# Kernel tuning notes

Hardware: AMD Instinct MI355X
Metric: run time of the kernel (lower is better)

Reference implementation:

```python
import jax, jax.numpy as jnp
import numpy as np

B, F, H, T = 32, 128, 256, 2048


def setup_inputs() -> dict:
    key = jax.random.key(0)
    ks = jax.random.split(key, 20)
    s = 0.05
    x = jax.random.normal(ks[0], (B, 1, T, F), dtype=jnp.float32)
    mask = (jax.random.uniform(ks[1], (B, 1, T, F)) < 0.5).astype(jnp.float32)
    delta = jax.random.uniform(ks[2], (B, 1, T, F), dtype=jnp.float32)  # time since last obs
    inp = jnp.concatenate([x, mask, delta], axis=1)  # [B, 3, T, F]
    p = lambda k, shape: jax.random.normal(k, shape, dtype=jnp.float32) * s
    return {
        "input": inp,
        "x_mean": p(ks[3], (F,)),
        # layer 0: input decay (diagonal), hidden decay, gates
        "w_dx": p(ks[4], (F,)), "b_dx": p(ks[5], (F,)),
        "W_dh0": p(ks[6], (F, H)), "b_dh0": p(ks[7], (H,)),
        "W0": p(ks[8], (F, 3 * H)), "U0": p(ks[9], (H, 3 * H)),
        "V0": p(ks[10], (F, 3 * H)), "b0": p(ks[11], (3 * H,)),
        # layer 1: hidden decay from delta, gates (input = prev layer hidden)
        "W_dh1": p(ks[12], (F, H)), "b_dh1": p(ks[13], (H,)),
        "W1": p(ks[14], (H, 3 * H)), "U1": p(ks[15], (H, 3 * H)),
        "V1": p(ks[16], (F, 3 * H)), "b1": p(ks[17], (3 * H,)),
    }


def _grud_cell(x_in, m, delta, h, W_dh, b_dh, W, U, V, b):
    # hidden-state decay from delta-time
    gamma_h = jnp.exp(-jax.nn.relu(delta @ W_dh + b_dh))  # [B,H]
    h = gamma_h * h
    pre = x_in @ W + m @ V + b                             # [B,3H]
    hU = h @ U[:, : 2 * H]                                 # r,z recurrent terms
    r = jax.nn.sigmoid(pre[:, :H] + hU[:, :H])
    z = jax.nn.sigmoid(pre[:, H : 2 * H] + hU[:, H : 2 * H])
    h_tilde = jnp.tanh(pre[:, 2 * H :] + (r * h) @ U[:, 2 * H :])
    return (1.0 - z) * h + z * h_tilde


def reference(input, x_mean, w_dx, b_dx, W_dh0, b_dh0, W0, U0, V0, b0,
              W_dh1, b_dh1, W1, U1, V1, b1):
    xs = jnp.moveaxis(input, 2, 0)  # [T, B, 3, F]
    x_last0 = jnp.broadcast_to(x_mean, (B, F))
    h0 = jnp.zeros((B, H), dtype=input.dtype)
    h1 = jnp.zeros((B, H), dtype=input.dtype)

    def step(carry, inp_t):
        x_last, h0, h1 = carry
        x, m, delta = inp_t[:, 0], inp_t[:, 1], inp_t[:, 2]  # [B,F] each
        # input decay toward empirical mean (GRU-D imputation)
        gamma_x = jnp.exp(-jax.nn.relu(delta * w_dx + b_dx))
        x_hat = m * x + (1.0 - m) * (gamma_x * x_last + (1.0 - gamma_x) * x_mean)
        h0n = _grud_cell(x_hat, m, delta, h0, W_dh0, b_dh0, W0, U0, V0, b0)
        h1n = _grud_cell(h0n, m, delta, h1, W_dh1, b_dh1, W1, U1, V1, b1)
        x_last_new = jnp.where(m > 0, x, x_last)  # update AFTER the cells, as in torch
        return (x_last_new, h0n, h1n), h1n

    _, ys = jax.lax.scan(step, (x_last0, h0, h1), xs)
    return ys  # [T, B, H]
```

## Files before the change

### kernel.cpp

```cpp
#include <hip/hip_runtime.h>

typedef _Float16 f16;
typedef _Float16 f16x2 __attribute__((ext_vector_type(2)));
typedef unsigned int u32;

#define CB 32
#define CF 128
#define CH 256
#define CT 2048
#define TCC 128
#define SEG 16
#define SLEN 128
#define SHBYTES 150784

static __device__ __forceinline__ f16x2 bc(u32 u){ return __builtin_bit_cast(f16x2, u); }
static __device__ __forceinline__ u32 packh2(float lo, float hi){ f16x2 v; v.x=(f16)lo; v.y=(f16)hi; return __builtin_bit_cast(u32, v); }

static __device__ __forceinline__ float dot2f(f16x2 a, f16x2 b, float c){
#if defined(__has_builtin)
#if __has_builtin(__builtin_amdgcn_fdot2)
  return __builtin_amdgcn_fdot2(a, b, c, false);
#else
  return c + (float)a.x*(float)b.x + (float)a.y*(float)b.y;
#endif
#else
  return c + (float)a.x*(float)b.x + (float)a.y*(float)b.y;
#endif
}
static __device__ __forceinline__ float dot4q(float acc, uint4 w, uint4 h){
  acc = dot2f(bc(w.x), bc(h.x), acc);
  acc = dot2f(bc(w.y), bc(h.y), acc);
  acc = dot2f(bc(w.z), bc(h.z), acc);
  acc = dot2f(bc(w.w), bc(h.w), acc);
  return acc;
}
#define DOT4V(ACC, BASE, H) { \
  ACC = dot2f(bc(wv[(BASE)+0]), bc((H).x), ACC); \
  ACC = dot2f(bc(wv[(BASE)+1]), bc((H).y), ACC); \
  ACC = dot2f(bc(wv[(BASE)+2]), bc((H).z), ACC); \
  ACC = dot2f(bc(wv[(BASE)+3]), bc((H).w), ACC); }

__global__ void init_hst(float* hst){
  int i = blockIdx.x*256 + threadIdx.x;
  if (i < 2*CB*CH) hst[i] = 0.f;
}

static __device__ __forceinline__ float wc0src(int k, int n, const float* W0, const float* V0, const float* Wdh0){
  if (k < 128) return (n < 768) ? W0[k*768 + n] : 0.f;
  if (k < 256) return (n < 768) ? V0[(k-128)*768 + n] : 0.f;
  return (n >= 768) ? Wdh0[(k-256)*256 + (n-768)] : 0.f;
}
static __device__ __forceinline__ float wc1src(int k, int n, const float* W1, const float* V1, const float* Wdh1){
  if (k < 256) return (n < 768) ? W1[k*768 + n] : 0.f;
  if (k < 384) return (n < 768) ? V1[(k-256)*768 + n] : 0.f;
  return (n >= 768) ? Wdh1[(k-384)*256 + (n-768)] : 0.f;
}
static __device__ __forceinline__ u32 wrz_pair(int flat, int jj, int L, const float* U){
  int p = L >> 2, q = L & 3;
  int cc = flat >> 3, j = flat & 7;
  int col = 4*p + cc;
  int pr = 32*q + 4*j + jj;
  return packh2(U[(2*pr)*768 + col], U[(2*pr+1)*768 + col]);
}
static __device__ __forceinline__ u32 wcc_pair(int flat, int jj, int L, const float* U){
  int p = L >> 2, q = L & 3;
  int cc2 = flat >> 3, j = flat & 7;
  int col = 512 + 2*p + cc2;
  int pr = 32*q + 4*j + jj;
  return packh2(U[(2*pr)*768 + col], U[(2*pr+1)*768 + col]);
}
static __device__ __forceinline__ u32 wrv_src(int v, int L, const float* U){
  if (v < 56) return wrz_pair(v >> 2, v & 3, L, U);
  if (v < 88){ int u = v - 56; return wcc_pair(u >> 2, u & 3, L, U); }
  int u = v - 88;
  return wrz_pair(26 + (u >> 2), u & 3, L, U);
}
static __device__ __forceinline__ u32 wrl_src(int g, int jj, int L, const float* U){
  if (g < 12) return wrz_pair(14 + g, jj, L, U);
  return wcc_pair(8 + (g - 12), jj, L, U);
}
static __device__ __forceinline__ u32 wrg_src(int g, int jj, int L, const float* U){
  if (g < 3) return wrz_pair(29 + g, jj, L, U);
  return wcc_pair(14 + (g - 3), jj, L, U);
}

__global__ __launch_bounds__(256) void pack_w(
    const float* __restrict__ W0, const float* __restrict__ V0, const float* __restrict__ Wdh0,
    const float* __restrict__ W1, const float* __restrict__ V1, const float* __restrict__ Wdh1,
    const float* __restrict__ U0, const float* __restrict__ U1,
    const float* __restrict__ b0, const float* __restrict__ bdh0,
    const float* __restrict__ b1, const float* __restrict__ bdh1,
    u32* __restrict__ WC0p, u32* __restrict__ WC1p,
    u32* __restrict__ WRVa, u32* __restrict__ WRVb,
    u32* __restrict__ WRLa, u32* __restrict__ WRLb,
    u32* __restrict__ WRGa, u32* __restrict__ WRGb,
    float* __restrict__ bias0, float* __restrict__ bias1){
  int idx = blockIdx.x*256 + threadIdx.x;
  if (idx < 196608){
    int k2 = idx >> 10, n = idx & 1023;
    WC0p[idx] = packh2(wc0src(2*k2, n, W0,V0,Wdh0), wc0src(2*k2+1, n, W0,V0,Wdh0));
  } else if (idx < 458752){
    int j = idx - 196608; int k2 = j >> 10, n = j & 1023;
    WC1p[j] = packh2(wc1src(2*k2, n, W1,V1,Wdh1), wc1src(2*k2+1, n, W1,V1,Wdh1));
  } else if (idx < 509952){
    int j = idx - 458752; int v = j >> 9, L = j & 511;
    WRVa[j] = wrv_src(v, L, U0);
  } else if (idx < 561152){
    int j = idx - 509952; int v = j >> 9, L = j & 511;
    WRVb[j] = wrv_src(v, L, U1);
  } else if (idx < 598016){
    int j = idx - 561152; int g = j >> 11, L = (j >> 2) & 511, jj = j & 3;
    WRLa[j] = wrl_src(g, jj, L, U0);
  } else if (idx < 634880){
    int j = idx - 598016; int g = j >> 11, L = (j >> 2) & 511, jj = j & 3;
    WRLb[j] = wrl_src(g, jj, L, U1);
  } else if (idx < 645120){
    int j = idx - 634880; int g = j >> 11, L = (j >> 2) & 511, jj = j & 3;
    WRGa[j] = wrg_src(g, jj, L, U0);
  } else if (idx < 655360){
    int j = idx - 645120; int g = j >> 11, L = (j >> 2) & 511, jj = j & 3;
    WRGb[j] = wrg_src(g, jj, L, U1);
  } else if (idx < 657408){
    int i = idx - 655360;
    if (i < 1024) bias0[i] = (i < 768) ? b0[i] : bdh0[i - 768];
    else { int j = i - 1024; bias1[j] = (j < 768) ? b1[j] : bdh1[j - 768]; }
  }
}

__global__ __launch_bounds__(256) void k1a(const float* __restrict__ in,
    float* __restrict__ segval, int* __restrict__ seghas){
  int tid = blockIdx.x*256 + threadIdx.x;
  int s = tid >> 12, chain = tid & 4095;
  int b = chain >> 7, f = chain & 127;
  const float* px = in + ((size_t)b*3 + 0)*CT*CF + f;
  const float* pm = in + ((size_t)b*3 + 1)*CT*CF + f;
  float last = 0.f; int has = 0;
  #pragma unroll 4
  for (int u = 0; u < SLEN; ++u){
    int t = s*SLEN + u;
    float m = pm[(size_t)t*CF], x = px[(size_t)t*CF];
    if (m > 0.f){ last = x; has = 1; }
  }
  segval[s*4096 + chain] = last;
  seghas[s*4096 + chain] = has;
}
__global__ __launch_bounds__(256) void k1b(const float* __restrict__ x_mean,
    const float* __restrict__ segval, const int* __restrict__ seghas, float* __restrict__ seed){
  int chain = blockIdx.x*256 + threadIdx.x;
  int f = chain & 127;
  float cur = x_mean[f];
  #pragma unroll
  for (int s = 0; s < SEG; ++s){
    seed[s*4096 + chain] = cur;
    if (seghas[s*4096 + chain]) cur = segval[s*4096 + chain];
  }
}
__global__ __launch_bounds__(256) void k1c(const float* __restrict__ in, const float* __restrict__ x_mean,
    const float* __restrict__ w_dx, const float* __restrict__ b_dx,
    const float* __restrict__ seed, f16* __restrict__ A){
  int tid = blockIdx.x*256 + threadIdx.x;
  int s = tid >> 12, chain = tid & 4095;
  int b = chain >> 7, f = chain & 127;
  const float wd = w_dx[f], bd = b_dx[f], xm = x_mean[f];
  const float* px = in + ((size_t)b*3 + 0)*CT*CF + f;
  const float* pm = in + ((size_t)b*3 + 1)*CT*CF + f;
  const float* pd = in + ((size_t)b*3 + 2)*CT*CF + f;
  float xl = seed[s*4096 + chain];
  #pragma unroll 4
  for (int u = 0; u < SLEN; ++u){
    int t = s*SLEN + u;
    float x = px[(size_t)t*CF], m = pm[(size_t)t*CF], d = pd[(size_t)t*CF];
    float gx = __expf(-fmaxf(d*wd + bd, 0.f));
    float xh = m*x + (1.f-m)*(gx*xl + (1.f-gx)*xm);
    f16* wq = A + ((size_t)t*CB + b)*384 + f;
    wq[0] = (f16)xh; wq[128] = (f16)m; wq[256] = (f16)d;
    xl = (m > 0.f) ? x : xl;
  }
}

static __device__ void gemm_tile(
    const u32* __restrict__ Aa, int lda, const u32* __restrict__ Ab, int ldb, int kasplit,
    int ktiles, const u32* __restrict__ Wp, const float* __restrict__ bias, float* __restrict__ Out,
    int row0, int n0, int tid, char* sm){
  u32 (*AsT)[68] = (u32 (*)[68])sm;
  u32 (*Bs)[64]  = (u32 (*)[64])(sm + 4352);
  const int tx = tid & 15, ty = tid >> 4;
  const int am = tid >> 2, akq = (tid & 3) * 4;
  const int bk = tid >> 4, bnq = (tid & 15) * 4;
  float acc[4][4] = {};
  for (int kt = 0; kt < ktiles; ++kt){
    int k2g = kt*16 + akq;
    uint4 ga;
    if (k2g < kasplit) ga = *(const uint4*)&Aa[(size_t)(row0 + am)*lda + k2g];
    else               ga = *(const uint4*)&Ab[(size_t)(row0 + am)*ldb + (k2g - kasplit)];
    uint4 gb = *(const uint4*)&Wp[(size_t)(kt*16 + bk)*1024 + n0 + bnq];
    __syncthreads();
    AsT[akq+0][am] = ga.x; AsT[akq+1][am] = ga.y; AsT[akq+2][am] = ga.z; AsT[akq+3][am] = ga.w;
    *(uint4*)&Bs[bk][bnq] = gb;
    __syncthreads();
    #pragma unroll
    for (int kk = 0; kk < 16; ++kk){
      uint4 bq = *(const uint4*)&Bs[kk][tx*4];
      uint4 aq = *(const uint4*)&AsT[kk][ty*4];
      f16x2 bv0 = bc(bq.x), bv1 = bc(bq.y), bv2 = bc(bq.z), bv3 = bc(bq.w);
      f16x2 av0 = bc(aq.x), av1 = bc(aq.y), av2 = bc(aq.z), av3 = bc(aq.w);
      acc[0][0] = dot2f(av0, bv0, acc[0][0]); acc[0][1] = dot2f(av0, bv1, acc[0][1]);
      acc[0][2] = dot2f(av0, bv2, acc[0][2]); acc[0][3] = dot2f(av0, bv3, acc[0][3]);
      acc[1][0] = dot2f(av1, bv0, acc[1][0]); acc[1][1] = dot2f(av1, bv1, acc[1][1]);
      acc[1][2] = dot2f(av1, bv2, acc[1][2]); acc[1][3] = dot2f(av1, bv3, acc[1][3]);
      acc[2][0] = dot2f(av2, bv0, acc[2][0]); acc[2][1] = dot2f(av2, bv1, acc[2][1]);
      acc[2][2] = dot2f(av2, bv2, acc[2][2]); acc[2][3] = dot2f(av2, bv3, acc[2][3]);
      acc[3][0] = dot2f(av3, bv0, acc[3][0]); acc[3][1] = dot2f(av3, bv1, acc[3][1]);
      acc[3][2] = dot2f(av3, bv2, acc[3][2]); acc[3][3] = dot2f(av3, bv3, acc[3][3]);
    }
  }
  const bool isg = (n0 >= 768);
  #pragma unroll
  for (int i = 0; i < 4; ++i){
    int r = row0 + ty*4 + i;
    int n = n0 + tx*4;
    float4 v;
    float* vv = (float*)&v;
    #pragma unroll
    for (int j = 0; j < 4; ++j){
      float x = acc[i][j] + bias[n + j];
      if (isg) x = __expf(-fmaxf(x, 0.f));
      vv[j] = x;
    }
    *(float4*)&Out[(size_t)r*1024 + n] = v;
  }
}

__global__ __launch_bounds__(512) void mega(
    const float* __restrict__ O0r, const float* __restrict__ O1r,
    const u32* __restrict__ WRVa, const u32* __restrict__ WRVb,
    const u32* __restrict__ WRLa, const u32* __restrict__ WRLb,
    const u32* __restrict__ WRGa, const u32* __restrict__ WRGb,
    float* __restrict__ hst, f16* __restrict__ h0cw, float* __restrict__ out,
    int t0_l1, int n0, int n1, int g0n, int g1n,
    const u32* __restrict__ g0a, float* __restrict__ g0out,
    const u32* __restrict__ g1a, const u32* __restrict__ g1b, float* __restrict__ g1out,
    const u32* __restrict__ WC0p, const u32* __restrict__ WC1p,
    const float* __restrict__ bias0, const float* __restrict__ bias1){
  extern __shared__ __align__(16) char smraw[];
  const int L = threadIdx.x;
  if (blockIdx.x >= 64){
    int gb = blockIdx.x - 64;
    int st = L >> 8, t2 = L & 255;
    char* smst = smraw + st*8448;
    if (gb < g0n){
      int tile = gb*2 + st;
      gemm_tile(g0a, 192, g0a, 192, 192, 12, WC0p, bias0, g0out, (tile>>4)*64, (tile&15)*64, t2, smst);
    } else {
      int tile = (gb - g0n)*2 + st;
      gemm_tile(g1a, 128, g1b, 192, 128, 16, WC1p, bias1, g1out, (tile>>4)*64, (tile&15)*64, t2, smst);
    }
    return;
  }
  const int role = blockIdx.x >> 5;
  const int b = blockIdx.x & 31;
  const int steps = role ? n1 : n0;
  if (steps == 0) return;
  const float* O = role ? O1r : O0r;
  const u32* WRV = role ? WRVb : WRVa;
  const u32* WRL = role ? WRLb : WRLa;
  const u32* WRG = role ? WRGb : WRGa;
  float* hcarry = hst + role*CB*CH;

  uint4* WL   = (uint4*)smraw;
  f16*  hdh_  = (f16*)(smraw + 147456);
  f16*  rh_   = (f16*)(smraw + 148096);
  float* hdf  = (float*)(smraw + 148736);
  float* zz   = (float*)(smraw + 149760);

  #pragma unroll
  for (int g = 0; g < 18; ++g) WL[g*512 + L] = *(const uint4*)&WRL[((size_t)g*512 + L)*4];
  u32 wv[100];
  #pragma unroll
  for (int i = 0; i < 100; ++i) wv[i] = WRV[i*512 + L];

  const int p = L >> 2, q = L & 3;
  size_t row = (size_t)b*1024;
  if (L < 256){
    float hd = O[row + 768 + L] * hcarry[b*256 + L];
    hdf[L] = hd; hdh_[(L>>6)*80 + (L&63)] = (f16)hd;
  }
  float prz = O[row + L];
  const int e2 = 2*p + (q & 1);
  float pc = (q < 2) ? O[row + 512 + e2] : 0.f;
  const char* hqb = (const char*)hdh_ + q*160;
  const char* rqb = (const char*)rh_ + q*160;
  __syncthreads();

  for (int lt = 0; lt < steps; ++lt){
    size_t nrow = row + (size_t)CB*1024;
    float nprz = 0.f, npc = 0.f, ngex = 0.f;
    if (lt + 1 < steps){
      nprz = O[nrow + L];
      if (q < 2){ npc = O[nrow + 512 + e2]; ngex = O[nrow + 768 + e2]; }
    }
    float a0=0.f, a1=0.f, a2=0.f, a3=0.f;
    #pragma unroll
    for (int j = 0; j < 8; ++j){
      uint4 h = ((const uint4*)hqb)[j];
      DOT4V(a0, 4*j, h);
      if (j < 6){ DOT4V(a1, 32 + 4*j, h); }
      else { uint4 wq = WL[(j-6)*512 + L]; a1 = dot4q(a1, wq, h); }
      { uint4 wq = WL[(2+j)*512 + L]; a2 = dot4q(a2, wq, h); }
      if (j < 2){ uint4 wq = WL[(10+j)*512 + L]; a3 = dot4q(a3, wq, h); }
      else if (j < 5){ DOT4V(a3, 88 + 4*(j-2), h); }
      else { uint4 wq = *(const uint4*)&WRG[((size_t)((j-5)*512) + L)*4]; a3 = dot4q(a3, wq, h); }
    }
    a0 += __shfl_xor(a0, 1); a1 += __shfl_xor(a1, 1); a2 += __shfl_xor(a2, 1); a3 += __shfl_xor(a3, 1);
    a0 += __shfl_xor(a0, 2); a1 += __shfl_xor(a1, 2); a2 += __shfl_xor(a2, 2); a3 += __shfl_xor(a3, 2);
    float sum1 = (q == 0) ? a0 : (q == 1) ? a1 : (q == 2) ? a2 : a3;
    float s1 = 1.f/(1.f + __expf(-(sum1 + prz)));
    if (L < 256) rh_[(L>>6)*80 + (L&63)] = (f16)(s1 * hdf[L]);
    else zz[L - 256] = s1;
    __syncthreads();
    float b0_=0.f, b1_=0.f;
    #pragma unroll
    for (int j = 0; j < 8; ++j){
      uint4 r = ((const uint4*)rqb)[j];
      DOT4V(b0_, 56 + 4*j, r);
      if (j < 6){ uint4 wq = WL[(12+j)*512 + L]; b1_ = dot4q(b1_, wq, r); }
      else { uint4 wq = *(const uint4*)&WRG[((size_t)((3+(j-6))*512) + L)*4]; b1_ = dot4q(b1_, wq, r); }
    }
    b0_ += __shfl_xor(b0_, 1); b1_ += __shfl_xor(b1_, 1);
    b0_ += __shfl_xor(b0_, 2); b1_ += __shfl_xor(b1_, 2);
    if (q < 2){
      float sumc = (q & 1) ? b1_ : b0_;
      float v = pc + sumc;
      float e = __expf(2.f*v);
      float ct = 1.f - 2.f/(1.f + e);
      float z = zz[e2];
      float hd = hdf[e2];
      float hn = hd + z*(ct - hd);
      float hdn = ngex*hn;
      hdf[e2] = hdn; hdh_[(e2>>6)*80 + (e2&63)] = (f16)hdn;
      if (role == 0) h0cw[((size_t)lt*CB + b)*256 + e2] = (f16)hn;
      else           out[((size_t)(t0_l1 + lt)*CB + b)*256 + e2] = hn;
      if (lt == steps-1) hcarry[b*256 + e2] = hn;
    }
    prz = nprz; pc = npc;
    row = nrow;
    __syncthreads();
  }
}

extern "C" void kernel_launch(void* const* d_in, const int* in_sizes, int n_in,
                              void* d_out, int out_size, void* d_ws, size_t ws_size,
                              hipStream_t stream){
  const float* input  = (const float*)d_in[0];
  const float* x_mean = (const float*)d_in[1];
  const float* w_dx   = (const float*)d_in[2];
  const float* b_dx   = (const float*)d_in[3];
  const float* Wdh0   = (const float*)d_in[4];
  const float* bdh0   = (const float*)d_in[5];
  const float* W0     = (const float*)d_in[6];
  const float* U0     = (const float*)d_in[7];
  const float* V0     = (const float*)d_in[8];
  const float* b0     = (const float*)d_in[9];
  const float* Wdh1   = (const float*)d_in[10];
  const float* bdh1   = (const float*)d_in[11];
  const float* W1     = (const float*)d_in[12];
  const float* U1     = (const float*)d_in[13];
  const float* V1     = (const float*)d_in[14];
  const float* b1     = (const float*)d_in[15];
  float* out = (float*)d_out;

  hipFuncSetAttribute((const void*)mega, hipFuncAttributeMaxDynamicSharedMemorySize, SHBYTES);

  char* base = (char*)d_ws;
  size_t off = 0;
  auto take = [&](size_t bytes)->char*{
    char* p = base + off;
    off = (off + bytes + 255) & ~(size_t)255;
    return p;
  };
  f16*  IN0h  = (f16*) take((size_t)CT*CB*384*2);
  u32*  WC0p  = (u32*) take((size_t)192*1024*4);
  u32*  WC1p  = (u32*) take((size_t)256*1024*4);
  u32*  WRVa  = (u32*) take((size_t)100*512*4);
  u32*  WRVb  = (u32*) take((size_t)100*512*4);
  u32*  WRLa  = (u32*) take((size_t)18*512*16);
  u32*  WRLb  = (u32*) take((size_t)18*512*16);
  u32*  WRGa  = (u32*) take((size_t)5*512*16);
  u32*  WRGb  = (u32*) take((size_t)5*512*16);
  float* bias0= (float*)take(1024*4);
  float* bias1= (float*)take(1024*4);
  float* hst  = (float*)take((size_t)2*CB*CH*4);
  float* segv = (float*)take((size_t)SEG*4096*4);
  int*   segh = (int*)  take((size_t)SEG*4096*4);
  float* seed = (float*)take((size_t)SEG*4096*4);
  float* O0b[2], *O1b[2]; f16* h0b[2];
  O0b[0] = (float*)take((size_t)TCC*CB*1024*4);
  O0b[1] = (float*)take((size_t)TCC*CB*1024*4);
  O1b[0] = (float*)take((size_t)TCC*CB*1024*4);
  O1b[1] = (float*)take((size_t)TCC*CB*1024*4);
  h0b[0] = (f16*)  take((size_t)TCC*CB*CH*2);
  h0b[1] = (f16*)  take((size_t)TCC*CB*CH*2);

  hipLaunchKernelGGL(init_hst, dim3(64), dim3(256), 0, stream, hst);
  hipLaunchKernelGGL(pack_w, dim3((657408 + 255)/256), dim3(256), 0, stream,
      W0, V0, Wdh0, W1, V1, Wdh1, U0, U1, b0, bdh0, b1, bdh1,
      WC0p, WC1p, WRVa, WRVb, WRLa, WRLb, WRGa, WRGb, bias0, bias1);
  hipLaunchKernelGGL(k1a, dim3(256), dim3(256), 0, stream, input, segv, segh);
  hipLaunchKernelGGL(k1b, dim3(16), dim3(256), 0, stream, x_mean, segv, segh, seed);
  hipLaunchKernelGGL(k1c, dim3(256), dim3(256), 0, stream, input, x_mean, w_dx, b_dx, seed, IN0h);

  const u32* IN0p = (const u32*)IN0h;
  const int nch = CT / TCC;
  for (int i = -1; i <= nch + 1; ++i){
    int r0 = (i >= 0 && i < nch) ? 1 : 0;
    int r1 = (i >= 2 && i < nch + 2) ? 1 : 0;
    int g0 = (i + 1 >= 0 && i + 1 < nch) ? 1 : 0;
    int g1 = (i - 1 >= 0 && i - 1 < nch) ? 1 : 0;
    int g0n = g0 ? 512 : 0, g1n = g1 ? 512 : 0;
    const float* O0r = O0b[i & 1];
    const float* O1r = O1b[i & 1];
    f16* h0cw = h0b[i & 1];
    const u32* g0a = IN0p + (size_t)(i+1)*TCC*CB*192;
    float* g0out = O0b[(i+1) & 1];
    const u32* g1a = (const u32*)h0b[(i-1) & 1];
    const u32* g1b = IN0p + (size_t)(i-1)*TCC*CB*192 + 64;
    float* g1out = O1b[(i-1) & 1];
    hipLaunchKernelGGL(mega, dim3(64 + g0n + g1n), dim3(512), SHBYTES, stream,
        O0r, O1r, WRVa, WRVb, WRLa, WRLb, WRGa, WRGb, hst, h0cw, out,
        (i-2)*TCC, r0 ? TCC : 0, r1 ? TCC : 0, g0n, g1n,
        g0a, g0out, g1a, g1b, g1out,
        WC0p, WC1p, bias0, bias1);
  }
}
```

Before: 3.848 ms.

## Hold all recurrent weights in registers and shrink LDS for two blocks per CU

```diff
diff --git a/kernel.cpp b/kernel.cpp
--- a/kernel.cpp
+++ b/kernel.cpp
@@ -11,7 +11,7 @@
 #define TCC 128
 #define SEG 16
 #define SLEN 128
-#define SHBYTES 150784
+#define SHBYTES 16896
 
 static __device__ __forceinline__ f16x2 bc(u32 u){ return __builtin_bit_cast(f16x2, u); }
 static __device__ __forceinline__ u32 packh2(float lo, float hi){ f16x2 v; v.x=(f16)lo; v.y=(f16)hi; return __builtin_bit_cast(u32, v); }
@@ -34,11 +34,6 @@
   acc = dot2f(bc(w.w), bc(h.w), acc);
   return acc;
 }
-#define DOT4V(ACC, BASE, H) { \
-  ACC = dot2f(bc(wv[(BASE)+0]), bc((H).x), ACC); \
-  ACC = dot2f(bc(wv[(BASE)+1]), bc((H).y), ACC); \
-  ACC = dot2f(bc(wv[(BASE)+2]), bc((H).z), ACC); \
-  ACC = dot2f(bc(wv[(BASE)+3]), bc((H).w), ACC); }
 
 __global__ void init_hst(float* hst){
   int i = blockIdx.x*256 + threadIdx.x;
@@ -68,20 +63,6 @@
   int col = 512 + 2*p + cc2;
   int pr = 32*q + 4*j + jj;
   return packh2(U[(2*pr)*768 + col], U[(2*pr+1)*768 + col]);
-}
-static __device__ __forceinline__ u32 wrv_src(int v, int L, const float* U){
-  if (v < 56) return wrz_pair(v >> 2, v & 3, L, U);
-  if (v < 88){ int u = v - 56; return wcc_pair(u >> 2, u & 3, L, U); }
-  int u = v - 88;
-  return wrz_pair(26 + (u >> 2), u & 3, L, U);
-}
-static __device__ __forceinline__ u32 wrl_src(int g, int jj, int L, const float* U){
-  if (g < 12) return wrz_pair(14 + g, jj, L, U);
-  return wcc_pair(8 + (g - 12), jj, L, U);
-}
-static __device__ __forceinline__ u32 wrg_src(int g, int jj, int L, const float* U){
-  if (g < 3) return wrz_pair(29 + g, jj, L, U);
-  return wcc_pair(14 + (g - 3), jj, L, U);
 }
 
 __global__ __launch_bounds__(256) void pack_w(
@@ -91,9 +72,8 @@
     const float* __restrict__ b0, const float* __restrict__ bdh0,
     const float* __restrict__ b1, const float* __restrict__ bdh1,
     u32* __restrict__ WC0p, u32* __restrict__ WC1p,
-    u32* __restrict__ WRVa, u32* __restrict__ WRVb,
-    u32* __restrict__ WRLa, u32* __restrict__ WRLb,
-    u32* __restrict__ WRGa, u32* __restrict__ WRGb,
+    u32* __restrict__ WRZa, u32* __restrict__ WRZb,
+    u32* __restrict__ WCCa, u32* __restrict__ WCCb,
     float* __restrict__ bias0, float* __restrict__ bias1){
   int idx = blockIdx.x*256 + threadIdx.x;
   if (idx < 196608){
@@ -102,24 +82,18 @@
   } else if (idx < 458752){
     int j = idx - 196608; int k2 = j >> 10, n = j & 1023;
     WC1p[j] = packh2(wc1src(2*k2, n, W1,V1,Wdh1), wc1src(2*k2+1, n, W1,V1,Wdh1));
-  } else if (idx < 509952){
-    int j = idx - 458752; int v = j >> 9, L = j & 511;
-    WRVa[j] = wrv_src(v, L, U0);
-  } else if (idx < 561152){
-    int j = idx - 509952; int v = j >> 9, L = j & 511;
-    WRVb[j] = wrv_src(v, L, U1);
-  } else if (idx < 598016){
-    int j = idx - 561152; int g = j >> 11, L = (j >> 2) & 511, jj = j & 3;
-    WRLa[j] = wrl_src(g, jj, L, U0);
-  } else if (idx < 634880){
-    int j = idx - 598016; int g = j >> 11, L = (j >> 2) & 511, jj = j & 3;
-    WRLb[j] = wrl_src(g, jj, L, U1);
-  } else if (idx < 645120){
-    int j = idx - 634880; int g = j >> 11, L = (j >> 2) & 511, jj = j & 3;
-    WRGa[j] = wrg_src(g, jj, L, U0);
+  } else if (idx < 524288){
+    int j = idx - 458752; int flat = j >> 11, L = (j >> 2) & 511, jj = j & 3;
+    WRZa[j] = wrz_pair(flat, jj, L, U0);
+  } else if (idx < 589824){
+    int j = idx - 524288; int flat = j >> 11, L = (j >> 2) & 511, jj = j & 3;
+    WRZb[j] = wrz_pair(flat, jj, L, U1);
+  } else if (idx < 622592){
+    int j = idx - 589824; int flat = j >> 11, L = (j >> 2) & 511, jj = j & 3;
+    WCCa[j] = wcc_pair(flat, jj, L, U0);
   } else if (idx < 655360){
-    int j = idx - 645120; int g = j >> 11, L = (j >> 2) & 511, jj = j & 3;
-    WRGb[j] = wrg_src(g, jj, L, U1);
+    int j = idx - 622592; int flat = j >> 11, L = (j >> 2) & 511, jj = j & 3;
+    WCCb[j] = wcc_pair(flat, jj, L, U1);
   } else if (idx < 657408){
     int i = idx - 655360;
     if (i < 1024) bias0[i] = (i < 768) ? b0[i] : bdh0[i - 768];
@@ -231,11 +205,10 @@
   }
 }
 
-__global__ __launch_bounds__(512) void mega(
+__global__ __launch_bounds__(512, 2) void mega(
     const float* __restrict__ O0r, const float* __restrict__ O1r,
-    const u32* __restrict__ WRVa, const u32* __restrict__ WRVb,
-    const u32* __restrict__ WRLa, const u32* __restrict__ WRLb,
-    const u32* __restrict__ WRGa, const u32* __restrict__ WRGb,
+    const u32* __restrict__ WRZa, const u32* __restrict__ WRZb,
+    const u32* __restrict__ WCCa, const u32* __restrict__ WCCb,
     float* __restrict__ hst, f16* __restrict__ h0cw, float* __restrict__ out,
     int t0_l1, int n0, int n1, int g0n, int g1n,
     const u32* __restrict__ g0a, float* __restrict__ g0out,
@@ -262,22 +235,21 @@
   const int steps = role ? n1 : n0;
   if (steps == 0) return;
   const float* O = role ? O1r : O0r;
-  const u32* WRV = role ? WRVb : WRVa;
-  const u32* WRL = role ? WRLb : WRLa;
-  const u32* WRG = role ? WRGb : WRGa;
+  const u32* WRZ = role ? WRZb : WRZa;
+  const u32* WCC = role ? WCCb : WCCa;
   float* hcarry = hst + role*CB*CH;
 
-  uint4* WL   = (uint4*)smraw;
-  f16*  hdh_  = (f16*)(smraw + 147456);
-  f16*  rh_   = (f16*)(smraw + 148096);
-  float* hdf  = (float*)(smraw + 148736);
-  float* zz   = (float*)(smraw + 149760);
-
+  f16*  hdh_  = (f16*)(smraw);
+  f16*  rh_   = (f16*)(smraw + 640);
+  float* hdf  = (float*)(smraw + 1280);
+  float* zz   = (float*)(smraw + 2304);
+
+  uint4 wrz[32];
   #pragma unroll
-  for (int g = 0; g < 18; ++g) WL[g*512 + L] = *(const uint4*)&WRL[((size_t)g*512 + L)*4];
-  u32 wv[100];
+  for (int i = 0; i < 32; ++i) wrz[i] = *(const uint4*)&WRZ[((size_t)i*512 + L)*4];
+  uint4 wcc[16];
   #pragma unroll
-  for (int i = 0; i < 100; ++i) wv[i] = WRV[i*512 + L];
+  for (int i = 0; i < 16; ++i) wcc[i] = *(const uint4*)&WCC[((size_t)i*512 + L)*4];
 
   const int p = L >> 2, q = L & 3;
   size_t row = (size_t)b*1024;
@@ -299,32 +271,31 @@
       nprz = O[nrow + L];
       if (q < 2){ npc = O[nrow + 512 + e2]; ngex = O[nrow + 768 + e2]; }
     }
+    float hdL = (L < 256) ? hdf[L] : 0.f;
+    float hd2 = hdf[e2];
     float a0=0.f, a1=0.f, a2=0.f, a3=0.f;
     #pragma unroll
     for (int j = 0; j < 8; ++j){
       uint4 h = ((const uint4*)hqb)[j];
-      DOT4V(a0, 4*j, h);
-      if (j < 6){ DOT4V(a1, 32 + 4*j, h); }
-      else { uint4 wq = WL[(j-6)*512 + L]; a1 = dot4q(a1, wq, h); }
-      { uint4 wq = WL[(2+j)*512 + L]; a2 = dot4q(a2, wq, h); }
-      if (j < 2){ uint4 wq = WL[(10+j)*512 + L]; a3 = dot4q(a3, wq, h); }
-      else if (j < 5){ DOT4V(a3, 88 + 4*(j-2), h); }
-      else { uint4 wq = *(const uint4*)&WRG[((size_t)((j-5)*512) + L)*4]; a3 = dot4q(a3, wq, h); }
+      a0 = dot4q(a0, wrz[j],      h);
+      a1 = dot4q(a1, wrz[8 + j],  h);
+      a2 = dot4q(a2, wrz[16 + j], h);
+      a3 = dot4q(a3, wrz[24 + j], h);
     }
     a0 += __shfl_xor(a0, 1); a1 += __shfl_xor(a1, 1); a2 += __shfl_xor(a2, 1); a3 += __shfl_xor(a3, 1);
     a0 += __shfl_xor(a0, 2); a1 += __shfl_xor(a1, 2); a2 += __shfl_xor(a2, 2); a3 += __shfl_xor(a3, 2);
     float sum1 = (q == 0) ? a0 : (q == 1) ? a1 : (q == 2) ? a2 : a3;
     float s1 = 1.f/(1.f + __expf(-(sum1 + prz)));
-    if (L < 256) rh_[(L>>6)*80 + (L&63)] = (f16)(s1 * hdf[L]);
+    if (L < 256) rh_[(L>>6)*80 + (L&63)] = (f16)(s1 * hdL);
     else zz[L - 256] = s1;
     __syncthreads();
+    float z = zz[e2];
     float b0_=0.f, b1_=0.f;
     #pragma unroll
     for (int j = 0; j < 8; ++j){
       uint4 r = ((const uint4*)rqb)[j];
-      DOT4V(b0_, 56 + 4*j, r);
-      if (j < 6){ uint4 wq = WL[(12+j)*512 + L]; b1_ = dot4q(b1_, wq, r); }
-      else { uint4 wq = *(const uint4*)&WRG[((size_t)((3+(j-6))*512) + L)*4]; b1_ = dot4q(b1_, wq, r); }
+      b0_ = dot4q(b0_, wcc[j],     r);
+      b1_ = dot4q(b1_, wcc[8 + j], r);
     }
     b0_ += __shfl_xor(b0_, 1); b1_ += __shfl_xor(b1_, 1);
     b0_ += __shfl_xor(b0_, 2); b1_ += __shfl_xor(b1_, 2);
@@ -333,8 +304,7 @@
       float v = pc + sumc;
       float e = __expf(2.f*v);
       float ct = 1.f - 2.f/(1.f + e);
-      float z = zz[e2];
-      float hd = hdf[e2];
+      float hd = hd2;
       float hn = hd + z*(ct - hd);
       float hdn = ngex*hn;
       hdf[e2] = hdn; hdh_[(e2>>6)*80 + (e2&63)] = (f16)hdn;
@@ -381,12 +351,10 @@
   f16*  IN0h  = (f16*) take((size_t)CT*CB*384*2);
   u32*  WC0p  = (u32*) take((size_t)192*1024*4);
   u32*  WC1p  = (u32*) take((size_t)256*1024*4);
-  u32*  WRVa  = (u32*) take((size_t)100*512*4);
-  u32*  WRVb  = (u32*) take((size_t)100*512*4);
-  u32*  WRLa  = (u32*) take((size_t)18*512*16);
-  u32*  WRLb  = (u32*) take((size_t)18*512*16);
-  u32*  WRGa  = (u32*) take((size_t)5*512*16);
-  u32*  WRGb  = (u32*) take((size_t)5*512*16);
+  u32*  WRZa  = (u32*) take((size_t)32*512*4*4);
+  u32*  WRZb  = (u32*) take((size_t)32*512*4*4);
+  u32*  WCCa  = (u32*) take((size_t)16*512*4*4);
+  u32*  WCCb  = (u32*) take((size_t)16*512*4*4);
   float* bias0= (float*)take(1024*4);
   float* bias1= (float*)take(1024*4);
   float* hst  = (float*)take((size_t)2*CB*CH*4);
@@ -404,7 +372,7 @@
   hipLaunchKernelGGL(init_hst, dim3(64), dim3(256), 0, stream, hst);
   hipLaunchKernelGGL(pack_w, dim3((657408 + 255)/256), dim3(256), 0, stream,
       W0, V0, Wdh0, W1, V1, Wdh1, U0, U1, b0, bdh0, b1, bdh1,
-      WC0p, WC1p, WRVa, WRVb, WRLa, WRLb, WRGa, WRGb, bias0, bias1);
+      WC0p, WC1p, WRZa, WRZb, WCCa, WCCb, bias0, bias1);
   hipLaunchKernelGGL(k1a, dim3(256), dim3(256), 0, stream, input, segv, segh);
   hipLaunchKernelGGL(k1b, dim3(16), dim3(256), 0, stream, x_mean, segv, segh, seed);
   hipLaunchKernelGGL(k1c, dim3(256), dim3(256), 0, stream, input, x_mean, w_dx, b_dx, seed, IN0h);
@@ -426,7 +394,7 @@
     const u32* g1b = IN0p + (size_t)(i-1)*TCC*CB*192 + 64;
     float* g1out = O1b[(i-1) & 1];
     hipLaunchKernelGGL(mega, dim3(64 + g0n + g1n), dim3(512), SHBYTES, stream,
-        O0r, O1r, WRVa, WRVb, WRLa, WRLb, WRGa, WRGb, hst, h0cw, out,
+        O0r, O1r, WRZa, WRZb, WCCa, WCCb, hst, h0cw, out,
         (i-2)*TCC, r0 ? TCC : 0, r1 ? TCC : 0, g0n, g1n,
         g0a, g0out, g1a, g1b, g1out,
         WC0p, WC1p, bias0, bias1);
```

New measurement: 4.010 ms. 1.04x slower.
